# Optimization experiments

Measured on AMD Instinct MI355X. Metric: run time of the kernel, lower is better.

Reference implementation:

```python
import jax, jax.numpy as jnp
import numpy as np
from jax import lax

NEG = -1e9


def cyk(scores, lens):
    """Inside algorithm (logsumexp semiring) for a span tree-CRF.
    scores: [B, N, N]; scores[b, i, j] = potential of right-closed span [i, j].
    lens:   [B] int sentence lengths.
    Returns logZ[b] = inside score of span [0, lens[b]-1].
    Chart A[b, i, w] = inside score of span starting at i with width w.
    Recurrence: A[i, w] = D[i, w] + logsumexp_{u=1..w-1}(A[i, u] + A[i+u, w-u]).
    """
    B, N = scores.shape[0], scores.shape[1]
    i = jnp.arange(N)
    u = jnp.arange(N + 1)
    # D[b, i, w] = scores[b, i, i+w-1] (span of width w starting at i)
    j_end = jnp.clip(i[:, None] + u[None, :] - 1, 0, N - 1)          # [N, N+1]
    D = jnp.take_along_axis(scores, j_end[None], axis=2)             # [B, N, N+1]
    valid_span = (u[None, :] >= 1) & (i[:, None] + u[None, :] <= N)  # [N, N+1]
    D = jnp.where(valid_span[None], D, NEG)

    A = jnp.full((B, N, N + 1), NEG, scores.dtype)
    A = A.at[:, :, 1].set(D[:, :, 1])  # width-1 spans
    rowc = jnp.clip(i[:, None] + u[None, :], 0, N - 1)               # [N, N+1]

    def step(A, w):
        colc = jnp.broadcast_to(jnp.clip(w - u, 0, N), (N, N + 1))
        right = A[:, rowc, colc]                                     # A[b, i+u, w-u]
        ok = (u[None, :] >= 1) & (u[None, :] <= w - 1) & (i[:, None] + u[None, :] <= N - 1)
        tmp = jnp.where(ok[None], A + right, NEG)                    # splits over u
        new = jax.nn.logsumexp(tmp, axis=-1) + D[:, :, w]
        return A.at[:, :, w].set(new), None

    A, _ = lax.scan(step, A, jnp.arange(2, N + 1))
    return jnp.take_along_axis(A[:, 0, :], lens[:, None], axis=1)[:, 0]


def setup_inputs() -> dict:
    key = jax.random.key(0)
    k1, k2 = jax.random.split(key)
    B, N = 64, 256
    span_logits = jax.random.normal(k1, (B, N, N, 2), jnp.float32)
    spans_ind = jax.random.randint(k2, (B, N, N), 0, 3).astype(jnp.int32)
    maskspan = jnp.ones((B, N, N), bool)
    span_mask = jnp.zeros((B, N, N), bool)
    return {"span_logits": span_logits, "spans_ind": spans_ind,
            "maskspan": maskspan, "span_mask": span_mask}


def reference(span_logits, spans_ind, maskspan, span_mask):
    # spans_ind: values>0 shifted down by 1, then to bool (gold span indicator)
    sind = jnp.where(spans_ind > 0, spans_ind - 1, spans_ind).astype(bool)
    # hard masking path (smoothing == 1.0, norm == False, ent_lamb == 0.0)
    s0 = jnp.where(span_mask | sind, NEG, span_logits[..., 0])
    s1 = jnp.where(span_mask | ~sind, NEG, span_logits[..., 1])
    ob = jnp.logaddexp(s0, s1)                                  # gold-constrained potentials
    allv = jnp.logaddexp(span_logits[..., 0], span_logits[..., 1])  # unconstrained
    lens = maskspan[:, 0].sum(-1).astype(jnp.int32)
    marginals = cyk(ob, lens)
    logz = cyk(allv, lens)
    return (logz - marginals).sum() / maskspan[:, 0].sum().astype(span_logits.dtype)
```

## Files before the change

### kernel.cpp

```cpp
#include <hip/hip_runtime.h>


#define NN 256
#define BATCH 64
#define NCHART (2 * BATCH)
#define NEGV -1000000000.0f
#define NEGB -1.0e30f
#define K2f 1.4426950408889634f
#define LN2f 0.6931471805599453f

#define CM_OFF  32896
#define BB_OFF  (CM_OFF + 257)
#define FLG_OFF (BB_OFF + 16)
#define MSC_OFF (FLG_OFF + 257)
#define S0_OFF  (MSC_OFF + 3)
#define S1_OFF  (S0_OFF + 3696)
#define LDSF    (S1_OFF + 3824)

#define RES_OFF ((size_t)16)
#define LEN_OFF ((size_t)(16 + NCHART))
#define FB_OFF  ((size_t)(16 + NCHART + BATCH + 16))

__device__ __forceinline__ float fexp2(float x) {
#if __has_builtin(__builtin_amdgcn_exp2f)
    return __builtin_amdgcn_exp2f(x);
#else
    return exp2f(x);
#endif
}

__device__ __forceinline__ float wave_max64(float x) {
    int v = __float_as_int(x);
    int s;
    s = __builtin_amdgcn_update_dpp(v, v, 0x111, 0xf, 0xf, false);
    v = __float_as_int(fmaxf(__int_as_float(v), __int_as_float(s)));
    s = __builtin_amdgcn_update_dpp(v, v, 0x112, 0xf, 0xf, false);
    v = __float_as_int(fmaxf(__int_as_float(v), __int_as_float(s)));
    s = __builtin_amdgcn_update_dpp(v, v, 0x114, 0xf, 0xf, false);
    v = __float_as_int(fmaxf(__int_as_float(v), __int_as_float(s)));
    s = __builtin_amdgcn_update_dpp(v, v, 0x118, 0xf, 0xf, false);
    v = __float_as_int(fmaxf(__int_as_float(v), __int_as_float(s)));
    s = __builtin_amdgcn_update_dpp(v, v, 0x142, 0xa, 0xf, false);
    v = __float_as_int(fmaxf(__int_as_float(v), __int_as_float(s)));
    s = __builtin_amdgcn_update_dpp(v, v, 0x143, 0xc, 0xf, false);
    v = __float_as_int(fmaxf(__int_as_float(v), __int_as_float(s)));
    return __int_as_float(__builtin_amdgcn_readlane(v, 63));
}

__device__ __forceinline__ float rlane(float v, int idx) {
    return __int_as_float(__builtin_amdgcn_readlane(__float_as_int(v), idx));
}

__device__ __forceinline__ int cstart(int v) {
    return 257 * (v - 1) - ((v * (v - 1)) >> 1);
}

__device__ __forceinline__ float score_at(const float* __restrict__ logits,
                                          const int* __restrict__ spans_ind,
                                          const void* __restrict__ span_mask,
                                          int isb, int t, int b, int i, int j) {
    size_t sidx = ((size_t)b * NN + i) * NN + j;
    float l0 = logits[2 * sidx];
    float l1 = logits[2 * sidx + 1];
    if (t) {
        float mx = fmaxf(l0, l1), mn = fminf(l0, l1);
        return mx + log1pf(__expf(mn - mx));
    } else {
        bool sind = (spans_ind[sidx] == 2);
        bool sm = isb ? (((const unsigned char*)span_mask)[sidx] != 0)
                      : (((const int*)span_mask)[sidx] != 0);
        float s0 = (sm || sind)  ? NEGV : l0;
        float s1 = (sm || !sind) ? NEGV : l1;
        float mx = fmaxf(s0, s1), mn = fminf(s0, s1);
        return mx + log1pf(__expf(mn - mx));
    }
}

template <int KK, int KK2>
__device__ __forceinline__ void group_olap(
    float* __restrict__ Lc, float* __restrict__ cm, int* flg, int* msc,
    const float* __restrict__ scrR, float* __restrict__ scrW,
    const float* __restrict__ bbR, float* __restrict__ bbW,
    int W, int wave, int lane, int lenv) {
    const int ESR = 257 - W;

    if (wave >= 8) {
        if constexpr (KK2 > 0) {
            const int W2 = W + 8;
            const int ESW = 257 - W2;
            const int p = (wave - 8) >> 1, sp = (wave - 8) & 1;
            const int G0 = 2 * p, G1 = G0 + 1;
            const int L0 = W2 + G0, L1 = W2 + G1;
            const bool has1 = (L1 <= 256);
            const int E0 = 257 - L0;
            const int E1 = has1 ? (257 - L1) : 0;
            const int lo0 = G0 + 9, hi = W2 - 9;

            float b0 = NEGB, b1 = NEGB;
            for (int uu = lo0 + lane; uu <= hi; uu += 64) {
                float cu = cm[uu];
                b0 = fmaxf(b0, cu + cm[L0 - uu]);
                if (uu >= lo0 + 1) b1 = fmaxf(b1, cu + cm[L1 - uu]);
            }
            b0 = wave_max64(b0);
            b1 = wave_max64(b1);
            if (lane == 0 && sp == 0) { bbW[G0] = b0; bbW[G1] = b1; }

            const int n = hi - lo0 + 1;
            if (n > 0) {
                const int C = (n + 1) >> 1;
                const int ua = lo0 + sp * C;
                const int ub = min(ua + C - 1, hi);
                const int R = ub - ua + 1;

                float su0r, su1r;
                {
                    int u = ua + lane;
                    int uc = (u <= ub) ? u : ub;
                    bool v0 = (lane < R);
                    bool v1 = v0 && has1 && (uc >= lo0 + 1);
                    float e0 = fexp2(cm[uc] + cm[L0 - uc] - b0);
                    float e1 = fexp2(cm[uc] + cm[L1 - uc] - b1);
                    su0r = v0 ? e0 : 0.f;
                    su1r = v1 ? e1 : 0.f;
                }
                float su2r = 0.f, su3r = 0.f;
                if (R > 64) {
                    int u = ua + 64 + lane;
                    int uc = (u <= ub) ? u : ub;
                    bool v0 = (64 + lane < R);
                    bool v1 = v0 && has1;
                    float e0 = fexp2(cm[uc] + cm[L0 - uc] - b0);
                    float e1 = fexp2(cm[uc] + cm[L1 - uc] - b1);
                    su2r = v0 ? e0 : 0.f;
                    su3r = v1 ? e1 : 0.f;
                }

                float a0[KK2], a1[KK2];
#pragma unroll
                for (int k = 0; k < KK2; ++k) { a0[k] = 0.f; a1[k] = 0.f; }

                if (R > 0) {
                    int la  = cstart(ua) + lane;
                    int ra0 = cstart(L0 - ua) + ua + lane;
                    int ra1 = cstart(L1 - ua) + ua + lane;
                    int A  = 257 - ua;
                    int B0 = 257 - (L0 - ua);
                    int B1 = 257 - (L1 - ua);
                    const int R0 = (R < 64) ? R : 64;
#pragma unroll 2
                    for (int idx = 0; idx < R0; ++idx) {
                        float su0 = rlane(su0r, idx);
                        float su1 = rlane(su1r, idx);
#pragma unroll
                        for (int k = 0; k < KK2; ++k) {
                            float lv = Lc[la  + 64 * k];
                            float r0 = Lc[ra0 + 64 * k];
                            float r1 = Lc[ra1 + 64 * k];
                            a0[k] = fmaf(su0 * lv, r0, a0[k]);
                            a1[k] = fmaf(su1 * lv, r1, a1[k]);
                        }
                        la += A; A -= 1;
                        ra0 -= B0; B0 += 1;
                        ra1 -= B1; B1 += 1;
                    }
#pragma unroll 2
                    for (int idx = 64; idx < R; ++idx) {
                        float su0 = rlane(su2r, idx - 64);
                        float su1 = rlane(su3r, idx - 64);
#pragma unroll
                        for (int k = 0; k < KK2; ++k) {
                            float lv = Lc[la  + 64 * k];
                            float r0 = Lc[ra0 + 64 * k];
                            float r1 = Lc[ra1 + 64 * k];
                            a0[k] = fmaf(su0 * lv, r0, a0[k]);
                            a1[k] = fmaf(su1 * lv, r1, a1[k]);
                        }
                        la += A; A -= 1;
                        ra0 -= B0; B0 += 1;
                        ra1 -= B1; B1 += 1;
                    }
                }
#pragma unroll
                for (int k = 0; k < KK2; ++k) {
                    int ge = lane + 64 * k;
                    if (ge < E0) scrW[(2 * G0 + sp) * ESW + ge] = a0[k];
                    if (ge < E1) scrW[(2 * G1 + sp) * ESW + ge] = a1[k];
                }
            }
        }
    } else {
        const int g = wave;
        const int L = W + g;
        if (L <= 256) {
            const int E = 257 - L;
            float m = NEGB;
            float s[KK];
#pragma unroll
            for (int k = 0; k < KK; ++k) s[k] = 0.f;

            if (W >= g + 18) {
                m = bbR[g];
#pragma unroll
                for (int k = 0; k < KK; ++k) {
                    int ge = lane + 64 * k;
                    if (ge < E)
                        s[k] = scrR[(2 * g) * ESR + ge] +
                               scrR[(2 * g + 1) * ESR + ge];
                }
            }

            const int b1lo = g + 1, b1hi = min(g + 8, W - 1);
            const int b2lo = max(W - 8, g + 9), b2hi = W - 1;
            float m2 = m;
            for (int u = b1lo; u <= b1hi; ++u) m2 = fmaxf(m2, cm[u] + cm[L - u]);
            for (int u = b2lo; u <= b2hi; ++u) m2 = fmaxf(m2, cm[u] + cm[L - u]);
            {
                float sc = fexp2(m - m2);
#pragma unroll
                for (int k = 0; k < KK; ++k) s[k] *= sc;
                m = m2;
            }
            for (int u = b1lo; u <= b1hi; ++u) {
                float su = fexp2(cm[u] + cm[L - u] - m);
                const int ca = cstart(u), cb = cstart(L - u);
#pragma unroll
                for (int k = 0; k < KK; ++k) {
                    int ge = lane + 64 * k;
                    if (ge < E)
                        s[k] = fmaf(su * Lc[ca + ge], Lc[cb + ge + u], s[k]);
                }
            }
            for (int u = b2lo; u <= b2hi; ++u) {
                float su = fexp2(cm[u] + cm[L - u] - m);
                const int ca = cstart(u), cb = cstart(L - u);
#pragma unroll
                for (int k = 0; k < KK; ++k) {
                    int ge = lane + 64 * k;
                    if (ge < E)
                        s[k] = fmaf(su * Lc[ca + ge], Lc[cb + ge + u], s[k]);
                }
            }

            for (int j = g; j >= 1; --j) {
                const int v = L - j;
                while (((volatile int*)flg)[v] == 0) {}
                asm volatile("" ::: "memory");
                float pm = cm[j] + cm[v];
                float nm = fmaxf(m, pm);
                float sc = fexp2(m - nm), pj = fexp2(pm - nm);
                const int cj = cstart(j), cl = cstart(v);
#pragma unroll
                for (int k = 0; k < KK; ++k) {
                    int ge = lane + 64 * k;
                    if (ge < E) {
                        float tt = Lc[cj + ge] * Lc[cl + ge + j] +
                                   Lc[cl + ge] * Lc[cj + ge + v];
                        s[k] = fmaf(s[k], sc, pj * tt);
                    }
                }
                m = nm;
            }

            float xa[KK];
            float mx = NEGB;
#pragma unroll
            for (int k = 0; k < KK; ++k) {
                int ge = lane + 64 * k;
                float av = NEGB;
                if (ge < E) av = Lc[cstart(L) + ge] + m + __log2f(s[k]);
                xa[k] = av;
                mx = fmaxf(mx, av);
            }
            mx = wave_max64(mx);
#pragma unroll
            for (int k = 0; k < KK; ++k) {
                int ge = lane + 64 * k;
                if (ge < E) Lc[cstart(L) + ge] = fexp2(xa[k] - mx);
            }
            if (lane == 0) {
                cm[L] = mx;
                if (L == lenv) ((float*)msc)[2] = xa[0];
            }
            __threadfence_block();
            asm volatile("" ::: "memory");
            if (lane == 0) ((volatile int*)flg)[L] = 1;
        }
    }
    __syncthreads();
}

__device__ __forceinline__ void level_direct(
    float* __restrict__ Lc, float* __restrict__ cm,
    float* __restrict__ swm, int* msc,
    int w, int tid, int wave, int lane, int lenv) {
    const int E = NN + 1 - w;
    float a = NEGB;
    if (tid < E) {
        float b0 = NEGB;
        for (int u = 1; u <= w - 1; ++u) b0 = fmaxf(b0, cm[u] + cm[w - u]);
        float s = 0.f;
        for (int u = 1; u <= w - 1; ++u) {
            float su = fexp2(cm[u] + cm[w - u] - b0);
            s = fmaf(su * Lc[cstart(u) + tid], Lc[cstart(w - u) + u + tid], s);
        }
        int ad = cstart(w) + tid;
        a = Lc[ad] + b0 + __log2f(s);
        Lc[ad] = a;
        if (tid == 0 && w == lenv) ((float*)msc)[2] = a;
    }
    float m = wave_max64(a);
    if (lane == 0) swm[wave] = m;
    __syncthreads();
    float cmw = swm[0];
#pragma unroll
    for (int i = 1; i < 16; ++i) cmw = fmaxf(cmw, swm[i]);
    if (tid < E) {
        int ad = cstart(w) + tid;
        Lc[ad] = fexp2(Lc[ad] - cmw);
    }
    if (tid == 0) cm[w] = cmw;
    __syncthreads();
}

template <bool USE_LDS>
__global__ __launch_bounds__(1024) void cyk_kernel(
    const float* __restrict__ logits,
    const int* __restrict__ spans_ind,
    const void* __restrict__ maskspan,
    const void* __restrict__ span_mask,
    float* __restrict__ ws) {
    extern __shared__ float lds[];
    const int c = blockIdx.x;
    const int b = c >> 1;
    const int t = c & 1;
    const int tid = threadIdx.x;
    const int wave = tid >> 6, lane = tid & 63;

    float* __restrict__ Lc = USE_LDS ? lds : (ws + FB_OFF + (size_t)c * LDSF);
    float* __restrict__ cm = Lc + CM_OFF;
    float* __restrict__ BB = Lc + BB_OFF;
    int* flg = (int*)(Lc + FLG_OFF);
    int* msc = (int*)(Lc + MSC_OFF);
    float* __restrict__ S0 = Lc + S0_OFF;
    float* __restrict__ S1 = Lc + S1_OFF;

    if (tid == 0) {
        ((float*)msc)[2] = K2f * NEGV;
        unsigned probe = *(const unsigned*)maskspan;
        msc[1] = (probe > 1u) ? 1 : 0;
    }
    if (tid < 257) flg[tid] = 0;
    __syncthreads();
    const int isb = msc[1];

    if (wave == 0) {
        int cnt = 0;
        for (int q = 0; q < 4; ++q) {
            int j = lane * 4 + q;
            size_t off = (size_t)b * NN * NN + j;
            int v = isb ? (((const unsigned char*)maskspan)[off] ? 1 : 0)
                        : (((const int*)maskspan)[off] ? 1 : 0);
            cnt += v;
        }
        for (int d = 32; d; d >>= 1) cnt += __shfl_xor(cnt, d);
        if (lane == 0) msc[0] = cnt;
    }

    for (int it = 0; it < 64; ++it) {
        int f = (it << 10) + tid;
        int i = f >> 8, j = f & 255;
        if (j >= i) {
            float sc = score_at(logits, spans_ind, span_mask, isb, t, b, i, j);
            Lc[cstart(j - i + 1) + i] = K2f * sc;
        }
    }
    __syncthreads();
    const int lenv = msc[0];

    {
        float a = (tid < NN) ? Lc[tid] : NEGB;
        if (tid == 0 && lenv == 1) ((float*)msc)[2] = a;
        float m = wave_max64(a);
        if (lane == 0) BB[wave] = m;
        __syncthreads();
        float c1 = BB[0];
#pragma unroll
        for (int i = 1; i < 16; ++i) c1 = fmaxf(c1, BB[i]);
        if (tid < NN) Lc[tid] = fexp2(a - c1);
        if (tid == 0) cm[1] = c1;
    }
    __syncthreads();

    for (int w = 2; w <= 9; ++w)
        level_direct(Lc, cm, BB, msc, w, tid, wave, lane, lenv);

#define GRP(KA, KB, WV)                                                     \
    {                                                                       \
        const int gk = ((WV) - 10) >> 3;                                    \
        const float* sR = (gk & 1) ? S1 : S0;                               \
        float* sW = (gk & 1) ? S0 : S1;                                     \
        const float* bR = BB + (gk & 1) * 8;                                \
        float* bW = BB + ((gk + 1) & 1) * 8;                                \
        group_olap<KA, KB>(Lc, cm, flg, msc, sR, sW, bR, bW, (WV),          \
                           wave, lane, lenv);                               \
    }
    for (int W = 10; W <= 50; W += 8) GRP(4, 4, W)
    GRP(4, 3, 58)
    for (int W = 66; W <= 114; W += 8) GRP(3, 3, W)
    GRP(3, 2, 122)
    for (int W = 130; W <= 178; W += 8) GRP(2, 2, W)
    GRP(2, 1, 186)
    for (int W = 194; W <= 242; W += 8) GRP(1, 1, W)
    GRP(1, 0, 250)
#undef GRP

    if (tid == 0) {
        int len = msc[0];
        float rres = (len >= 1) ? (((float*)msc)[2] * LN2f) : NEGV;
        ws[RES_OFF + c] = rres;
        if (t == 0) ws[LEN_OFF + b] = (float)len;
    }
}

__global__ __launch_bounds__(64) void finish_kernel(const float* __restrict__ ws,
                                                    float* __restrict__ out) {
    int b = threadIdx.x;
    float diff = ws[RES_OFF + 2 * b + 1] - ws[RES_OFF + 2 * b];
    float len  = ws[LEN_OFF + b];
    for (int d = 32; d > 0; d >>= 1) {
        diff += __shfl_xor(diff, d);
        len  += __shfl_xor(len, d);
    }
    if (b == 0) out[0] = diff / len;
}

extern "C" void kernel_launch(void* const* d_in, const int* in_sizes, int n_in,
                              void* d_out, int out_size, void* d_ws, size_t ws_size,
                              hipStream_t stream) {
    const float* logits    = (const float*)d_in[0];
    const int*   spans_ind = (const int*)d_in[1];
    const void*  maskspan  = d_in[2];
    const void*  span_mask = d_in[3];
    float* ws = (float*)d_ws;

    const size_t shbytes = (size_t)LDSF * sizeof(float);
    hipError_t e = hipFuncSetAttribute(
        reinterpret_cast<const void*>(&cyk_kernel<true>),
        hipFuncAttributeMaxDynamicSharedMemorySize, (int)shbytes);
    if (e == hipSuccess) {
        hipLaunchKernelGGL(cyk_kernel<true>, dim3(NCHART), dim3(1024), shbytes,
                           stream, logits, spans_ind, maskspan, span_mask, ws);
    } else {
        hipLaunchKernelGGL(cyk_kernel<false>, dim3(NCHART), dim3(1024), 0,
                           stream, logits, spans_ind, maskspan, span_mask, ws);
    }
    hipLaunchKernelGGL(finish_kernel, dim3(1), dim3(64), 0, stream,
                       ws, (float*)d_out);
}
```

Measured before the change: 420.9 us.

## Replace per-level block barriers for widths 2-9 with flag-synchronized wave seeding

Widths 2 through 9 were computed one level at a time, each with two block-wide barriers and a block max reduction. Now each of eight waves owns one width and waits on per-level LDS flags, using symmetric split pairing and an online rescaled sum, so the early levels can overlap. The group loop also prefetches the already-ready operands before spinning on the flag, and score computation moves to base-2 log/exp directly. The cost is spin-waiting and a per-wave instead of block-wide normalization max.

```diff
diff --git a/kernel.cpp b/kernel.cpp
--- a/kernel.cpp
+++ b/kernel.cpp
@@ -55,25 +55,77 @@
     return 257 * (v - 1) - ((v * (v - 1)) >> 1);
 }
 
-__device__ __forceinline__ float score_at(const float* __restrict__ logits,
-                                          const int* __restrict__ spans_ind,
-                                          const void* __restrict__ span_mask,
-                                          int isb, int t, int b, int i, int j) {
+__device__ __forceinline__ float score2_at(const float* __restrict__ logits,
+                                           const int* __restrict__ spans_ind,
+                                           const void* __restrict__ span_mask,
+                                           int isb, int t, int b, int i, int j) {
     size_t sidx = ((size_t)b * NN + i) * NN + j;
     float l0 = logits[2 * sidx];
     float l1 = logits[2 * sidx + 1];
+    float mx, mn;
     if (t) {
-        float mx = fmaxf(l0, l1), mn = fminf(l0, l1);
-        return mx + log1pf(__expf(mn - mx));
+        mx = fmaxf(l0, l1); mn = fminf(l0, l1);
     } else {
         bool sind = (spans_ind[sidx] == 2);
         bool sm = isb ? (((const unsigned char*)span_mask)[sidx] != 0)
                       : (((const int*)span_mask)[sidx] != 0);
         float s0 = (sm || sind)  ? NEGV : l0;
         float s1 = (sm || !sind) ? NEGV : l1;
-        float mx = fmaxf(s0, s1), mn = fminf(s0, s1);
-        return mx + log1pf(__expf(mn - mx));
-    }
+        mx = fmaxf(s0, s1); mn = fminf(s0, s1);
+    }
+    return fmaf(K2f, mx, __log2f(1.f + fexp2(K2f * (mn - mx))));
+}
+
+__device__ __forceinline__ void seed_levels(
+    float* __restrict__ Lc, float* __restrict__ cm, int* flg, int* msc,
+    int wave, int lane, int lenv) {
+    if (wave >= 8) return;
+    const int L = wave + 2;
+    const int E = 257 - L;
+    float m = NEGB;
+    float s[4] = {0.f, 0.f, 0.f, 0.f};
+    for (int j = L >> 1; j >= 1; --j) {
+        const int v = L - j;
+        if (v >= 2) { while (((volatile int*)flg)[v] == 0) {} }
+        asm volatile("" ::: "memory");
+        float pm = cm[j] + cm[v];
+        float nm = fmaxf(m, pm);
+        float sc = fexp2(m - nm), pj = fexp2(pm - nm);
+        const int cj = cstart(j), cl = cstart(v);
+#pragma unroll
+        for (int k = 0; k < 4; ++k) {
+            int ge = lane + 64 * k;
+            if (ge < E) {
+                float tt = Lc[cj + ge] * Lc[cl + ge + j];
+                if (j != v) tt += Lc[cl + ge] * Lc[cj + ge + v];
+                s[k] = fmaf(s[k], sc, pj * tt);
+            }
+        }
+        m = nm;
+    }
+    float xa[4];
+    float mx = NEGB;
+#pragma unroll
+    for (int k = 0; k < 4; ++k) {
+        int ge = lane + 64 * k;
+        float av = NEGB;
+        if (ge < E) av = Lc[cstart(L) + ge] + m + __log2f(s[k]);
+        xa[k] = av;
+        mx = fmaxf(mx, av);
+    }
+    mx = wave_max64(mx);
+#pragma unroll
+    for (int k = 0; k < 4; ++k) {
+        int ge = lane + 64 * k;
+        if (ge < E) Lc[cstart(L) + ge] = fexp2(xa[k] - mx);
+    }
+    if (lane == 0) {
+        cm[L] = mx;
+        if (L == lenv) ((float*)msc)[2] = xa[0];
+    }
+    __threadfence_block();
+    asm volatile("" ::: "memory");
+    if (lane == 0) ((volatile int*)flg)[L] = 1;
 }
 
 template <int KK, int KK2>
@@ -244,18 +296,26 @@
 
             for (int j = g; j >= 1; --j) {
                 const int v = L - j;
+                const int cj = cstart(j), cl = cstart(v);
+                float xj0[KK], xj1[KK];
+#pragma unroll
+                for (int k = 0; k < KK; ++k) {
+                    int ge = lane + 64 * k;
+                    xj0[k] = (ge < E) ? Lc[cj + ge] : 0.f;
+                    xj1[k] = (ge < E) ? Lc[cj + ge + v] : 0.f;
+                }
+                asm volatile("" ::: "memory");
                 while (((volatile int*)flg)[v] == 0) {}
                 asm volatile("" ::: "memory");
                 float pm = cm[j] + cm[v];
                 float nm = fmaxf(m, pm);
                 float sc = fexp2(m - nm), pj = fexp2(pm - nm);
-                const int cj = cstart(j), cl = cstart(v);
 #pragma unroll
                 for (int k = 0; k < KK; ++k) {
                     int ge = lane + 64 * k;
                     if (ge < E) {
-                        float tt = Lc[cj + ge] * Lc[cl + ge + j] +
-                                   Lc[cl + ge] * Lc[cj + ge + v];
+                        float tt = xj0[k] * Lc[cl + ge + j] +
+                                   Lc[cl + ge] * xj1[k];
                         s[k] = fmaf(s[k], sc, pj * tt);
                     }
                 }
@@ -287,39 +347,6 @@
             if (lane == 0) ((volatile int*)flg)[L] = 1;
         }
     }
-    __syncthreads();
-}
-
-__device__ __forceinline__ void level_direct(
-    float* __restrict__ Lc, float* __restrict__ cm,
-    float* __restrict__ swm, int* msc,
-    int w, int tid, int wave, int lane, int lenv) {
-    const int E = NN + 1 - w;
-    float a = NEGB;
-    if (tid < E) {
-        float b0 = NEGB;
-        for (int u = 1; u <= w - 1; ++u) b0 = fmaxf(b0, cm[u] + cm[w - u]);
-        float s = 0.f;
-        for (int u = 1; u <= w - 1; ++u) {
-            float su = fexp2(cm[u] + cm[w - u] - b0);
-            s = fmaf(su * Lc[cstart(u) + tid], Lc[cstart(w - u) + u + tid], s);
-        }
-        int ad = cstart(w) + tid;
-        a = Lc[ad] + b0 + __log2f(s);
-        Lc[ad] = a;
-        if (tid == 0 && w == lenv) ((float*)msc)[2] = a;
-    }
-    float m = wave_max64(a);
-    if (lane == 0) swm[wave] = m;
-    __syncthreads();
-    float cmw = swm[0];
-#pragma unroll
-    for (int i = 1; i < 16; ++i) cmw = fmaxf(cmw, swm[i]);
-    if (tid < E) {
-        int ad = cstart(w) + tid;
-        Lc[ad] = fexp2(Lc[ad] - cmw);
-    }
-    if (tid == 0) cm[w] = cmw;
     __syncthreads();
 }
 
@@ -371,8 +398,8 @@
         int f = (it << 10) + tid;
         int i = f >> 8, j = f & 255;
         if (j >= i) {
-            float sc = score_at(logits, spans_ind, span_mask, isb, t, b, i, j);
-            Lc[cstart(j - i + 1) + i] = K2f * sc;
+            Lc[cstart(j - i + 1) + i] =
+                score2_at(logits, spans_ind, span_mask, isb, t, b, i, j);
         }
     }
     __syncthreads();
@@ -392,8 +419,8 @@
     }
     __syncthreads();
 
-    for (int w = 2; w <= 9; ++w)
-        level_direct(Lc, cm, BB, msc, w, tid, wave, lane, lenv);
+    seed_levels(Lc, cm, flg, msc, wave, lane, lenv);
+    __syncthreads();
 
 #define GRP(KA, KB, WV)                                                     \
     {                                                                       \
```

Measured after the change: 393.7 us. 6.5% less time.
